# Optimization experiments

Hardware: AMD Instinct MI355X
Metric: run time of the kernel (lower is better)

## Reference

```python
import jax, jax.numpy as jnp
import numpy as np

WEIGHT = 10.0
# illegal[i, j] == True  iff transition (i -> j) is illegal; from {(0,2),(1,0),(2,0),(2,1)}
_ILLEGAL = np.zeros((3, 3), dtype=bool)
for _i, _j in [(0, 2), (1, 0), (2, 0), (2, 1)]:
    _ILLEGAL[_i, _j] = True


def setup_inputs() -> dict:
    key = jax.random.key(0)
    phase_logits = jax.random.normal(key, (2048, 8192, 3), dtype=jnp.float32)
    return {"phase_logits": phase_logits}


def reference(phase_logits):
    B, T, C = phase_logits.shape
    illegal = jnp.asarray(_ILLEGAL)
    pred = jnp.argmax(phase_logits, axis=-1)          # [B, T]
    pt = pred[:, :-1]                                  # phase at t     [B, T-1]
    pt1 = pred[:, 1:]                                  # phase at t+1   [B, T-1]
    mask = illegal[pt, pt1]                            # [B, T-1] bool
    # logit of the (argmax) illegal phase at t+1: phase_logits[b, t+1, pt1]
    gathered = jnp.take_along_axis(phase_logits[:, 1:, :], pt1[..., None], axis=-1)[..., 0]
    loss = jnp.sum(jnp.where(mask, gathered * gathered, jnp.zeros_like(gathered)))
    count = jnp.sum(mask.astype(phase_logits.dtype))
    return jnp.where(count > 0, WEIGHT * loss / count, jnp.zeros_like(loss))
```

## Files before the change

### kernel.cpp

```cpp
#include <hip/hip_runtime.h>


#define NTHREADS  256
#define SLAB      2048
#define JITER     8
#define TLEN      8192

struct alignas(4) F3 { float a, b, c; };

__device__ __forceinline__ F3 load_f3(const float* __restrict__ p) {
    F3 v;
    __builtin_memcpy(&v, p, sizeof(F3));
    return v;
}

__device__ __forceinline__ int argmax3_pack(F3 v) {
    float bm = v.a; int bi = 0;
    if (v.b > bm) { bm = v.b; bi = 1; }
    if (v.c > bm) { bm = v.c; bi = 2; }
    return (__float_as_int(bm) & ~3) | bi;
}

__global__ __launch_bounds__(NTHREADS) void pcl_main(const float* __restrict__ x,
                                                     float* __restrict__ part_loss,
                                                     unsigned int* __restrict__ part_cnt) {
    const int tid  = threadIdx.x;
    const int lane = tid & 63;
    const int wv   = tid >> 6;
    const float* xb = x + (size_t)blockIdx.x * SLAB * 3;

    F3 own[JITER];
    #pragma unroll
    for (int j = 0; j < JITER; ++j)
        own[j] = load_f3(xb + (size_t)3 * (tid + j * NTHREADS));

    const bool has_next = ((blockIdx.x & 3u) != 3u);
    F3 nextv = own[0];
    if (tid == NTHREADS - 1 && has_next)
        nextv = load_f3(xb + (size_t)3 * SLAB);

    int pk[JITER];
    #pragma unroll
    for (int j = 0; j < JITER; ++j) pk[j] = argmax3_pack(own[j]);

    __shared__ int sm[4][JITER];
    if (lane == 0) {
        #pragma unroll
        for (int j = 0; j < JITER; ++j) sm[wv][j] = pk[j];
    }
    __syncthreads();

    float loss = 0.0f;
    unsigned int cnt = 0;
    #pragma unroll
    for (int j = 0; j < JITER; ++j) {
        int npk = __shfl_down(pk[j], 1, 64);
        if (lane == 63) {
            if (wv < 3)              npk = sm[wv + 1][j];
            else if (j < JITER - 1)  npk = sm[0][j + 1];
            else                     npk = argmax3_pack(nextv);
        }
        bool valid = !(wv == 3 && lane == 63 && j == JITER - 1 && !has_next);
        if (valid) {
            int code = (pk[j] & 3) * 3 + (npk & 3);
            if ((0xCC >> code) & 1) {
                float nmx = __int_as_float(npk & ~3);
                loss = fmaf(nmx, nmx, loss);
                cnt++;
            }
        }
    }

    #pragma unroll
    for (int off = 32; off > 0; off >>= 1) {
        loss += __shfl_down(loss, off, 64);
        cnt  += __shfl_down(cnt,  off, 64);
    }

    __shared__ float        sl[4];
    __shared__ unsigned int sc[4];
    if (lane == 0) { sl[wv] = loss; sc[wv] = cnt; }
    __syncthreads();

    if (tid == 0) {
        part_loss[blockIdx.x] = sl[0] + sl[1] + sl[2] + sl[3];
        part_cnt[blockIdx.x]  = sc[0] + sc[1] + sc[2] + sc[3];
    }
}

__global__ __launch_bounds__(NTHREADS) void pcl_final(const float* __restrict__ part_loss,
                                                      const unsigned int* __restrict__ part_cnt,
                                                      float* __restrict__ out, int npart) {
    double L = 0.0;
    unsigned int C = 0;
    for (int i = threadIdx.x; i < npart; i += NTHREADS) {
        L += (double)part_loss[i];
        C += part_cnt[i];
    }
    #pragma unroll
    for (int off = 32; off > 0; off >>= 1) {
        L += __shfl_down(L, off, 64);
        C += __shfl_down(C, off, 64);
    }
    __shared__ double       sl[4];
    __shared__ unsigned int sc[4];
    int lane = threadIdx.x & 63;
    int wid  = threadIdx.x >> 6;
    if (lane == 0) { sl[wid] = L; sc[wid] = C; }
    __syncthreads();
    if (threadIdx.x == 0) {
        double       Lt = sl[0] + sl[1] + sl[2] + sl[3];
        unsigned int Ct = sc[0] + sc[1] + sc[2] + sc[3];
        out[0] = (Ct > 0u) ? (float)(10.0 * Lt / (double)Ct) : 0.0f;
    }
}

extern "C" void kernel_launch(void* const* d_in, const int* in_sizes, int n_in,
                              void* d_out, int out_size, void* d_ws, size_t ws_size,
                              hipStream_t stream) {
    const float* x = (const float*)d_in[0];
    const int B = in_sizes[0] / (3 * TLEN);
    const int grid = B * (TLEN / SLAB);

    float*        part_loss = (float*)d_ws;
    unsigned int* part_cnt  = (unsigned int*)((char*)d_ws + (size_t)grid * sizeof(float));

    pcl_main<<<grid, NTHREADS, 0, stream>>>(x, part_loss, part_cnt);
    pcl_final<<<1, NTHREADS, 0, stream>>>(part_loss, part_cnt, (float*)d_out, grid);
}
```

Before: 274.7 us.

## Stage block slab through LDS with nontemporal float4 loads

Each block now copies its 2048x3 float slab into shared memory using coalesced 16-byte nontemporal loads, instead of every thread doing strided 12-byte scalar loads. Each thread then reads its current and next element from LDS, which removes the shuffle and cross-wave neighbor exchange. The argmax is computed twice per element and the kernel uses about 24KB of LDS per block, which may limit occupancy. The aim is better global-load efficiency on a bandwidth-bound kernel.

```diff
diff --git a/kernel.cpp b/kernel.cpp
--- a/kernel.cpp
+++ b/kernel.cpp
@@ -4,15 +4,12 @@
 #define NTHREADS  256
 #define SLAB      2048
 #define JITER     8
+#define F4_PER_BLK 1536
 #define TLEN      8192
 
-struct alignas(4) F3 { float a, b, c; };
+typedef float f4v __attribute__((ext_vector_type(4)));
 
-__device__ __forceinline__ F3 load_f3(const float* __restrict__ p) {
-    F3 v;
-    __builtin_memcpy(&v, p, sizeof(F3));
-    return v;
-}
+struct F3 { float a, b, c; };
 
 __device__ __forceinline__ int argmax3_pack(F3 v) {
     float bm = v.a; int bi = 0;
@@ -24,47 +21,35 @@
 __global__ __launch_bounds__(NTHREADS) void pcl_main(const float* __restrict__ x,
                                                      float* __restrict__ part_loss,
                                                      unsigned int* __restrict__ part_cnt) {
-    const int tid  = threadIdx.x;
-    const int lane = tid & 63;
-    const int wv   = tid >> 6;
-    const float* xb = x + (size_t)blockIdx.x * SLAB * 3;
+    const int tid = threadIdx.x;
+    __shared__ float sx[SLAB * 3 + 4];
 
-    F3 own[JITER];
+    const f4v* xb4 = (const f4v*)x + (size_t)blockIdx.x * F4_PER_BLK;
+    f4v* sx4 = (f4v*)sx;
     #pragma unroll
-    for (int j = 0; j < JITER; ++j)
-        own[j] = load_f3(xb + (size_t)3 * (tid + j * NTHREADS));
-
+    for (int j = 0; j < F4_PER_BLK / NTHREADS; ++j) {
+        int i = j * NTHREADS + tid;
+        sx4[i] = __builtin_nontemporal_load(xb4 + i);
+    }
     const bool has_next = ((blockIdx.x & 3u) != 3u);
-    F3 nextv = own[0];
-    if (tid == NTHREADS - 1 && has_next)
-        nextv = load_f3(xb + (size_t)3 * SLAB);
-
-    int pk[JITER];
-    #pragma unroll
-    for (int j = 0; j < JITER; ++j) pk[j] = argmax3_pack(own[j]);
-
-    __shared__ int sm[4][JITER];
-    if (lane == 0) {
-        #pragma unroll
-        for (int j = 0; j < JITER; ++j) sm[wv][j] = pk[j];
-    }
+    if (tid == 0 && has_next)
+        sx4[F4_PER_BLK] = __builtin_nontemporal_load(xb4 + F4_PER_BLK);
     __syncthreads();
 
     float loss = 0.0f;
     unsigned int cnt = 0;
     #pragma unroll
     for (int j = 0; j < JITER; ++j) {
-        int npk = __shfl_down(pk[j], 1, 64);
-        if (lane == 63) {
-            if (wv < 3)              npk = sm[wv + 1][j];
-            else if (j < JITER - 1)  npk = sm[0][j + 1];
-            else                     npk = argmax3_pack(nextv);
-        }
-        bool valid = !(wv == 3 && lane == 63 && j == JITER - 1 && !has_next);
+        int t = tid + j * NTHREADS;
+        F3 cur = *(const F3*)(sx + 3 * t);
+        F3 nxt = *(const F3*)(sx + 3 * t + 3);
+        bool valid = !(t == SLAB - 1 && !has_next);
         if (valid) {
-            int code = (pk[j] & 3) * 3 + (npk & 3);
+            int pc = argmax3_pack(cur);
+            int pn = argmax3_pack(nxt);
+            int code = (pc & 3) * 3 + (pn & 3);
             if ((0xCC >> code) & 1) {
-                float nmx = __int_as_float(npk & ~3);
+                float nmx = __int_as_float(pn & ~3);
                 loss = fmaf(nmx, nmx, loss);
                 cnt++;
             }
@@ -76,12 +61,11 @@
         loss += __shfl_down(loss, off, 64);
         cnt  += __shfl_down(cnt,  off, 64);
     }
-
     __shared__ float        sl[4];
     __shared__ unsigned int sc[4];
+    int lane = tid & 63, wv = tid >> 6;
     if (lane == 0) { sl[wv] = loss; sc[wv] = cnt; }
     __syncthreads();
-
     if (tid == 0) {
         part_loss[blockIdx.x] = sl[0] + sl[1] + sl[2] + sl[3];
         part_cnt[blockIdx.x]  = sc[0] + sc[1] + sc[2] + sc[3];
@@ -104,8 +88,7 @@
     }
     __shared__ double       sl[4];
     __shared__ unsigned int sc[4];
-    int lane = threadIdx.x & 63;
-    int wid  = threadIdx.x >> 6;
+    int lane = threadIdx.x & 63, wid = threadIdx.x >> 6;
     if (lane == 0) { sl[wid] = L; sc[wid] = C; }
     __syncthreads();
     if (threadIdx.x == 0) {
```

Measured after the change: 259.1 us. 5.7% less time.
